# Kernel optimization log

Measured on AMD Instinct MI355X. Metric: run time of the kernel, lower is better.

The kernel has to match this reference:

```python
import jax, jax.numpy as jnp
import numpy as np

D_MODEL = 1024
N_BLOCK = 20
EPS = 1e-8


def setup_inputs() -> dict:
    key = jax.random.key(0)
    k = jax.random.split(key, 7)
    B, S, D, NB = 8, 2048, D_MODEL, N_BLOCK
    e = jax.random.normal(k[0], (B, S, D), dtype=jnp.float32)
    m = jax.random.normal(k[1], (B, S, D), dtype=jnp.float32)
    state = jax.random.normal(k[2], (1, NB * D), dtype=jnp.float32)
    # learned params of the EntNet-style RNN_cell
    U = jax.random.normal(k[3], (D, D), dtype=jnp.float32) * 0.02
    V = jax.random.normal(k[4], (D, D), dtype=jnp.float32) * 0.02
    W = jax.random.normal(k[5], (D, D), dtype=jnp.float32) * 0.02
    keys = jax.random.normal(k[6], (NB, D), dtype=jnp.float32) * 0.02
    return {"e": e, "m": m, "state": state, "U": U, "V": V, "W": W, "keys": keys}


def reference(e, m, state, U, V, W, keys):
    B, S, D = e.shape
    NB = keys.shape[0]
    h0 = state.reshape(NB, D)  # shared initial memory state across batch
    x = e + m  # combined per-timestep input, (B, S, D)

    def step(h, xt):  # h: (NB, D), xt: (D,)
        # per-slot gate: content similarity + key similarity
        g = jax.nn.sigmoid(h @ xt + keys @ xt)  # (NB,)
        # candidate memory
        cand = jnp.tanh(h @ U.T + keys @ V.T + (W @ xt)[None, :])  # (NB, D)
        h = h + g[:, None] * cand
        # per-slot L2 normalization
        h = h / (jnp.linalg.norm(h, axis=1, keepdims=True) + EPS)
        return h, None

    def run(xseq):  # xseq: (S, D) -> final state (NB, D)
        hT, _ = jax.lax.scan(step, h0, xseq)
        return hT

    out = jax.vmap(run)(x)  # (B, NB, D)
    return out
```

## Files before the change

### kernel.cpp

```cpp
#include <hip/hip_runtime.h>
#include <cstdint>
#include <cstddef>

namespace {

constexpr int D   = 1024;
constexpr int NB  = 20;
constexpr int B   = 8;
constexpr int S   = 2048;
constexpr int NWG = 32;
constexpr float EPS = 1e-8f;

typedef __attribute__((ext_vector_type(4))) float f4_t;
typedef __attribute__((ext_vector_type(8))) short s8_t;
typedef unsigned long long u64_t;

__device__ __forceinline__ unsigned short f2bf(float f) {
  unsigned u = __float_as_uint(f);
  u += 0x7fffu + ((u >> 16) & 1u);
  return (unsigned short)(u >> 16);
}
__device__ __forceinline__ float bf2f(unsigned short h) {
  return __uint_as_float(((unsigned)h) << 16);
}
__device__ __forceinline__ float u64lo(u64_t x) { return __uint_as_float((unsigned)x); }
__device__ __forceinline__ float u64hi(u64_t x) { return __uint_as_float((unsigned)(x >> 32)); }
__device__ __forceinline__ float rcp_f(float x) { return __builtin_amdgcn_rcpf(x); }
__device__ __forceinline__ float sigm_fast(float x) { return rcp_f(1.0f + __expf(-x)); }
__device__ __forceinline__ float tanh_fast(float x) {
  const float e = __expf(2.0f * x);
  return 1.0f - 2.0f * rcp_f(e + 1.0f);
}

#define MFMA(a, b, c) __builtin_amdgcn_mfma_f32_16x16x32_bf16((a), (b), (c), 0, 0, 0)
#define ALOAD64(p) __hip_atomic_load((p), __ATOMIC_RELAXED, __HIP_MEMORY_SCOPE_AGENT)
#define ASTORE64(p, v) __hip_atomic_store((p), (v), __ATOMIC_RELAXED, __HIP_MEMORY_SCOPE_AGENT)
#define ALOAD32(p) __hip_atomic_load((p), __ATOMIC_RELAXED, __HIP_MEMORY_SCOPE_AGENT)
#define ASTORE32(p, v) __hip_atomic_store((p), (v), __ATOMIC_RELAXED, __HIP_MEMORY_SCOPE_AGENT)

constexpr size_t OFF_HBUF = 0;
constexpr size_t OFF_NORM = OFF_HBUF + 2ull * B * NB * 512 * 4;
constexpr size_t OFF_CTR  = OFF_NORM + 2ull * B * NB * NWG * 4;
constexpr size_t OFF_KV   = OFF_CTR + (size_t)B * 32 * 4;
constexpr size_t OFF_KX   = OFF_KV + (size_t)NB * D * 4;
constexpr size_t OFF_UHI  = OFF_KX + (size_t)B * S * NB * 4;
constexpr size_t OFF_ULO  = OFF_UHI + (size_t)D * D * 2;
constexpr size_t OFF_WHI  = OFF_ULO + (size_t)D * D * 2;
constexpr size_t OFF_WLO  = OFF_WHI + (size_t)D * D * 2;


__global__ void k_convert(const float* __restrict__ U, const float* __restrict__ W,
                          unsigned short* __restrict__ Uhi, unsigned short* __restrict__ Ulo,
                          unsigned short* __restrict__ Whi, unsigned short* __restrict__ Wlo) {
  const int n = D * D;
  for (int i = blockIdx.x * blockDim.x + threadIdx.x; i < n; i += gridDim.x * blockDim.x) {
    float u = U[i];
    unsigned short h = f2bf(u);
    Uhi[i] = h;
    Ulo[i] = f2bf(u - bf2f(h));
    float w = W[i];
    h = f2bf(w);
    Whi[i] = h;
    Wlo[i] = f2bf(w - bf2f(h));
  }
}

__global__ void k_kv(const float* __restrict__ keys, const float* __restrict__ V,
                     float* __restrict__ KV) {
  const int tid = threadIdx.x;
  const int j = blockIdx.x * 64 + (tid >> 2);
  const int kq = tid & 3;
  const f4_t* v4 = (const f4_t*)(V + (size_t)j * D + kq * 256);
  const f4_t* k4base = (const f4_t*)keys;
  float acc[NB];
#pragma unroll
  for (int i = 0; i < NB; ++i) acc[i] = 0.f;
  for (int q = 0; q < 64; ++q) {
    const f4_t v = v4[q];
#pragma unroll
    for (int i = 0; i < NB; ++i) {
      const f4_t kk = k4base[i * 256 + kq * 64 + q];
      acc[i] += kk[0] * v[0] + kk[1] * v[1] + kk[2] * v[2] + kk[3] * v[3];
    }
  }
#pragma unroll
  for (int i = 0; i < NB; ++i) {
    float s = acc[i];
    s += __shfl_xor(s, 1);
    s += __shfl_xor(s, 2);
    if (kq == 0) KV[(size_t)i * D + j] = s;
  }
}

__global__ void k_kx(const float* __restrict__ e, const float* __restrict__ m,
                     const float* __restrict__ keys, float* __restrict__ KX) {
  __shared__ f4_t xs[256];
  __shared__ float part[NB][8];
  const int bt = blockIdx.x, tid = threadIdx.x;
  xs[tid] = ((const f4_t*)e)[(size_t)bt * 256 + tid] + ((const f4_t*)m)[(size_t)bt * 256 + tid];
  __syncthreads();
  if (tid < 160) {
    const int i = tid >> 3, s8 = tid & 7;
    float acc = 0.f;
    const f4_t* k4 = (const f4_t*)keys + i * 256 + s8 * 32;
    for (int q = 0; q < 32; ++q) {
      const f4_t kk = k4[q];
      const f4_t xx = xs[s8 * 32 + q];
      acc += kk[0] * xx[0] + kk[1] * xx[1] + kk[2] * xx[2] + kk[3] * xx[3];
    }
    part[i][s8] = acc;
  }
  __syncthreads();
  if (tid < NB) {
    float s = 0.f;
#pragma unroll
    for (int q = 0; q < 8; ++q) s += part[tid][q];
    KX[(size_t)bt * NB + tid] = s;
  }
}

__global__ void k_state(const float* __restrict__ state, unsigned* __restrict__ Hbuf,
                        float* __restrict__ NormP, int* __restrict__ ctr) {
  const int idx = blockIdx.x * 256 + threadIdx.x;
  if (idx < B * NB * 512) {
    const int r = idx % (NB * 512);
    const int i = r >> 9, d2 = (r & 511) << 1;
    const unsigned short a = f2bf(state[i * D + d2]);
    const unsigned short c = f2bf(state[i * D + d2 + 1]);
    Hbuf[idx] = (unsigned)a | ((unsigned)c << 16);
  }
  const int j = idx - B * NB * 512;
  if (j >= 0 && j < B * NB * NWG) NormP[j] = 1.0f / 32.0f;
  const int q = idx - B * NB * 512 - B * NB * NWG;
  if (q >= 0 && q < B * 32) ctr[q] = 0;
}


struct __align__(16) LdsT {
  unsigned short hnA[NB * 1024];
  unsigned short xtA[2][1024];
  float credU[4][2][2][16][20];
  float wxAcc[4][2][16];
  float gAcc[4][2][16];
  float KVs[NB][32];
  float ownH[NB][32];
  float pad_force_1_block_per_cu[3072];
};

__device__ __forceinline__ void build_xt(unsigned short* xt , int tid, f4_t x) {
  const unsigned short h0 = f2bf(x[0]), h1 = f2bf(x[1]), h2 = f2bf(x[2]), h3 = f2bf(x[3]);
  const unsigned short u0 = f2bf(x[0] - bf2f(h0)), u1 = f2bf(x[1] - bf2f(h1));
  const unsigned short u2 = f2bf(x[2] - bf2f(h2)), u3 = f2bf(x[3] - bf2f(h3));
  const int kp = tid << 2;
  *(unsigned*)&xt[kp] = (unsigned)h0 | ((unsigned)h1 << 16);
  *(unsigned*)&xt[kp + 2] = (unsigned)h2 | ((unsigned)h3 << 16);
  *(unsigned*)&xt[1024 + kp] = (unsigned)u0 | ((unsigned)u1 << 16);
  *(unsigned*)&xt[1024 + kp + 2] = (unsigned)u2 | ((unsigned)u3 << 16);
}

__device__ __forceinline__ void stage_h(unsigned short* hn, int tid, const u64_t* hv) {
  const int blkk = tid >> 1;
  const int half = (tid & 1) << 2;
#pragma unroll
  for (int j = 0; j < 20; ++j)
    *(u64_t*)&hn[(j << 10) + ((blkk ^ (j & 15)) << 3) + half] = hv[j];
}

__device__ __forceinline__ void bar_lds() {
  asm volatile("s_waitcnt lgkmcnt(0)\n\ts_barrier" ::: "memory");
}
__device__ __forceinline__ void bar_full() {
  asm volatile("s_waitcnt vmcnt(0) lgkmcnt(0)\n\ts_barrier" ::: "memory");
}

__device__ __forceinline__ void poll32(const unsigned* fb, int ln31, int wg,
                                       unsigned tgt, unsigned pv) {
  if (__ballot(pv >= tgt) == ~0ull) return;
  for (;;) {
    const unsigned v = (ln31 == wg) ? tgt : ALOAD32(fb + ln31);
    if (__ballot(v >= tgt) == ~0ull) return;
    __builtin_amdgcn_s_sleep(1);
  }
}

__launch_bounds__(256, 1)
__global__ void k_rnn(const float* __restrict__ e, const float* __restrict__ m,
                      const float* __restrict__ state,
                      const float* __restrict__ KX, const float* __restrict__ KV,
                      const unsigned short* __restrict__ Uhi, const unsigned short* __restrict__ Ulo,
                      const unsigned short* __restrict__ Whi, const unsigned short* __restrict__ Wlo,
                      unsigned* __restrict__ Hbuf, float* __restrict__ NormP,
                      int* __restrict__ ctr, float* __restrict__ out) {
  __shared__ LdsT L;
  const int tid = threadIdx.x;
  const int b = blockIdx.x >> 5;
  const int wg = blockIdx.x & 31;
  const int wv = tid >> 6;
  const int ln = tid & 63;
  const int l15 = ln & 15;
  const int lo4 = ln >> 4;
  const int ln31 = tid & 31;
  unsigned* ctrp = (unsigned*)ctr + b * 32;

  const bool uact = (ln < 40);
  const int ui = wv * 5 + (ln >> 3);
  const int uc4 = (ln & 7) << 2;

  s8_t BUh[2][8], BUl[2][8], BWh[2][8], BWl[2][8];
  {
    const int rowb = (wg << 5) + l15;
#pragma unroll
    for (int nt = 0; nt < 2; ++nt)
#pragma unroll
      for (int kf = 0; kf < 8; ++kf) {
        const size_t off = (size_t)(rowb + nt * 16) * D + (wv << 8) + (kf << 5) + (lo4 << 3);
        BUh[nt][kf] = *(const s8_t*)(Uhi + off);
        BUl[nt][kf] = *(const s8_t*)(Ulo + off);
        BWh[nt][kf] = *(const s8_t*)(Whi + off);
        BWl[nt][kf] = *(const s8_t*)(Wlo + off);
      }
  }
  if (tid < 160) {
    const int i = tid >> 3, c4 = (tid & 7) << 2;
    *(f4_t*)&L.ownH[i][c4] = *(const f4_t*)(state + (size_t)i * D + (wg << 5) + c4);
    *(f4_t*)&L.KVs[i][c4] = *(const f4_t*)(KV + (size_t)i * D + (wg << 5) + c4);
  }

  f4_t evv, mvv;
  float sreg = 1.f;
  float kxreg = 0.f;

  s8_t AX[8];
  f4_t cWa0 = {0, 0, 0, 0}, cWa1 = {0, 0, 0, 0};

  {
    u64_t hv[20];
    const u64_t* hb8 = (const u64_t*)Hbuf + (size_t)(0 * B + b) * (NB * 256);
#pragma unroll
    for (int j = 0; j < 20; ++j) hv[j] = ALOAD64(hb8 + j * 256 + tid);
    const f4_t x0 = ((const f4_t*)e)[(size_t)(b * S) * 256 + tid] +
                    ((const f4_t*)m)[(size_t)(b * S) * 256 + tid];
    build_xt(&L.xtA[0][0], tid, x0);
    stage_h(L.hnA, tid, hv);
    if (uact) kxreg = KX[(size_t)(b * S) * NB + ui];
    evv = ((const f4_t*)e)[(size_t)(b * S + 1) * 256 + tid];
    mvv = ((const f4_t*)m)[(size_t)(b * S + 1) * 256 + tid];
    asm volatile("s_waitcnt lgkmcnt(0)" ::: "memory");
    const unsigned short* xb = &L.xtA[0][0];
#pragma unroll
    for (int kf = 0; kf < 8; ++kf) {
      const int blk = (wv << 5) + (kf << 2) + lo4;
      AX[kf] = *(const s8_t*)&xb[(l15 & 1) * 1024 + (blk << 3)];
    }
#pragma unroll
    for (int kf = 0; kf < 8; ++kf) {
      cWa0 = MFMA(AX[kf], BWh[0][kf], cWa0);
      cWa0 = MFMA(AX[kf], BWl[0][kf], cWa0);
      cWa1 = MFMA(AX[kf], BWh[1][kf], cWa1);
      cWa1 = MFMA(AX[kf], BWl[1][kf], cWa1);
    }
  }
  __syncthreads();

  for (int t = 0; t < S; ++t) {
    const int nxt2 = (t + 1) & 1;

    f4_t cU00 = {0, 0, 0, 0}, cU01 = {0, 0, 0, 0}, cU10 = {0, 0, 0, 0}, cU11 = {0, 0, 0, 0};
    f4_t cG0 = {0, 0, 0, 0}, cG1 = {0, 0, 0, 0};
    {
      const unsigned short* hb = L.hnA;
      const int r1 = 16 + (l15 < 4 ? l15 : 3);
      s8_t A0[8], A1[8];
#pragma unroll
      for (int kf = 0; kf < 8; ++kf) {
        const int blk = (wv << 5) + (kf << 2) + lo4;
        A0[kf] = *(const s8_t*)&hb[(l15 << 10) + ((blk ^ l15) << 3)];
        A1[kf] = *(const s8_t*)&hb[(r1 << 10) + ((blk ^ (r1 & 15)) << 3)];
      }
#pragma unroll
      for (int kf = 0; kf < 8; ++kf) {
        cU00 = MFMA(A0[kf], BUh[0][kf], cU00);
        cU00 = MFMA(A0[kf], BUl[0][kf], cU00);
        cU01 = MFMA(A0[kf], BUh[1][kf], cU01);
        cU01 = MFMA(A0[kf], BUl[1][kf], cU01);
        cU10 = MFMA(A1[kf], BUh[0][kf], cU10);
        cU10 = MFMA(A1[kf], BUl[0][kf], cU10);
        cU11 = MFMA(A1[kf], BUh[1][kf], cU11);
        cU11 = MFMA(A1[kf], BUl[1][kf], cU11);
        cG0 = MFMA(AX[kf], A0[kf], cG0);
        cG1 = MFMA(AX[kf], A1[kf], cG1);
      }
    }
#pragma unroll
    for (int q = 0; q < 4; ++q) {
      const int r = (lo4 << 2) + q;
      L.credU[wv][0][0][r][l15] = cU00[q];
      L.credU[wv][0][1][r][l15] = cU01[q];
      L.credU[wv][1][0][r][l15] = cU10[q];
      L.credU[wv][1][1][r][l15] = cU11[q];
    }
    if (lo4 == 0) {
      L.wxAcc[wv][0][l15] = cWa0[0] + cWa0[1];
      L.wxAcc[wv][1][l15] = cWa1[0] + cWa1[1];
      L.gAcc[wv][0][l15] = cG0[0] + cG0[1];
      L.gAcc[wv][1][l15] = cG1[0] + cG1[1];
    }
    bar_lds();

    unsigned pv = 0;
    if (t + 1 < S) pv = (ln31 == wg) ? (unsigned)(t + 1) : ALOAD32(ctrp + ln31);

    if (uact) {
      const int i = ui, c4 = uc4;
      const int mt = i >> 4, r = i & 15, nt = c4 >> 4, ccc = c4 & 15;
      const f4_t sU = *(const f4_t*)&L.credU[0][mt][nt][r][ccc] +
                      *(const f4_t*)&L.credU[1][mt][nt][r][ccc] +
                      *(const f4_t*)&L.credU[2][mt][nt][r][ccc] +
                      *(const f4_t*)&L.credU[3][mt][nt][r][ccc];
      const f4_t wx = *(const f4_t*)&L.wxAcc[0][nt][ccc] +
                      *(const f4_t*)&L.wxAcc[1][nt][ccc] +
                      *(const f4_t*)&L.wxAcc[2][nt][ccc] +
                      *(const f4_t*)&L.wxAcc[3][nt][ccc];
      const f4_t kv = *(const f4_t*)&L.KVs[i][c4];
      const f4_t oh = *(const f4_t*)&L.ownH[i][c4];
      const float s = sreg;
      const float gpre = s * (L.gAcc[0][mt][r] + L.gAcc[1][mt][r] +
                              L.gAcc[2][mt][r] + L.gAcc[3][mt][r]) + kxreg;
      const float g = sigm_fast(gpre);
      f4_t hn;
      float sq = 0.f;
#pragma unroll
      for (int u = 0; u < 4; ++u) {
        const float cand = tanh_fast(s * sU[u] + kv[u] + wx[u]);
        const float hx = s * oh[u] + g * cand;
        hn[u] = hx;
        sq += hx * hx;
      }
      *(f4_t*)&L.ownH[i][c4] = hn;
      const unsigned d0 = (unsigned)f2bf(hn[0]) | ((unsigned)f2bf(hn[1]) << 16);
      const unsigned d1 = (unsigned)f2bf(hn[2]) | ((unsigned)f2bf(hn[3]) << 16);
      u64_t* hb8 = (u64_t*)Hbuf + (size_t)(nxt2 * B + b) * (NB * 256) +
                   (i << 8) + (wg << 3) + (c4 >> 2);
      ASTORE64(hb8, (u64_t)d0 | ((u64_t)d1 << 32));
      sq += __shfl_xor(sq, 1);
      sq += __shfl_xor(sq, 2);
      sq += __shfl_xor(sq, 4);
      if ((ln & 7) == 0) {
        unsigned* np = (unsigned*)NormP + ((size_t)(nxt2 * B + b) * NB + i) * NWG + wg;
        ASTORE32(np, __float_as_uint(sq));
      }
    }
    bar_full();

    if (tid == 0) ASTORE32(ctrp + wg, (unsigned)(t + 1));

    if (t + 1 < S) {
      poll32(ctrp, ln31, wg, (unsigned)(t + 1), pv);
      u64_t hv[20];
      const u64_t* g0 = (const u64_t*)Hbuf + (size_t)(nxt2 * B + b) * (NB * 256);
#pragma unroll
      for (int j = 0; j < 20; ++j) hv[j] = ALOAD64(g0 + j * 256 + tid);
      float np0 = 0.f;
      if (uact) {
        const u64_t* n0 = (const u64_t*)NormP + ((size_t)(nxt2 * B + b) * NB + ui) * 16 + ((ln & 7) << 1);
        const u64_t a0 = ALOAD64(n0);
        const u64_t a1 = ALOAD64(n0 + 1);
        np0 = u64lo(a0) + u64hi(a0) + u64lo(a1) + u64hi(a1);
        kxreg = KX[((size_t)b * S + t + 1) * NB + ui];
      }
      asm volatile("" ::: "memory");
      build_xt(&L.xtA[0][0], tid, evv + mvv);
      asm volatile("s_waitcnt lgkmcnt(0)" ::: "memory");
      {
        const unsigned short* xb = &L.xtA[0][0];
#pragma unroll
        for (int kf = 0; kf < 8; ++kf) {
          const int blk = (wv << 5) + (kf << 2) + lo4;
          AX[kf] = *(const s8_t*)&xb[(l15 & 1) * 1024 + (blk << 3)];
        }
        cWa0 = (f4_t){0, 0, 0, 0};
        cWa1 = (f4_t){0, 0, 0, 0};
#pragma unroll
        for (int kf = 0; kf < 8; ++kf) {
          cWa0 = MFMA(AX[kf], BWh[0][kf], cWa0);
          cWa0 = MFMA(AX[kf], BWl[0][kf], cWa0);
          cWa1 = MFMA(AX[kf], BWh[1][kf], cWa1);
          cWa1 = MFMA(AX[kf], BWl[1][kf], cWa1);
        }
      }
      stage_h(L.hnA, tid, hv);
      if (t + 2 < S) {
        evv = ((const f4_t*)e)[(size_t)(b * S + t + 2) * 256 + tid];
        mvv = ((const f4_t*)m)[(size_t)(b * S + t + 2) * 256 + tid];
      }
      if (uact) {
        float s0 = np0;
        s0 += __shfl_xor(s0, 1);
        s0 += __shfl_xor(s0, 2);
        s0 += __shfl_xor(s0, 4);
        sreg = rcp_f(sqrtf(s0) + EPS);
      }
    }
    asm volatile("s_waitcnt lgkmcnt(0)" ::: "memory");
  }

  poll32(ctrp, ln31, wg, (unsigned)S, 0u);
  if (uact) {
    const int i = ui, c4 = uc4;
    const u64_t* np8 = (const u64_t*)NormP + ((size_t)(0 * B + b) * NB + i) * 16 + ((ln & 7) << 1);
    const u64_t x0 = ALOAD64(np8);
    const u64_t x1 = ALOAD64(np8 + 1);
    float sq = u64lo(x0) + u64hi(x0) + u64lo(x1) + u64hi(x1);
    sq += __shfl_xor(sq, 1);
    sq += __shfl_xor(sq, 2);
    sq += __shfl_xor(sq, 4);
    const float sc = rcp_f(sqrtf(sq) + EPS);
    const f4_t oh = *(const f4_t*)&L.ownH[i][c4];
    f4_t ov;
#pragma unroll
    for (int u = 0; u < 4; ++u) ov[u] = sc * oh[u];
    *(f4_t*)(out + (size_t)b * NB * D + (size_t)i * D + (wg << 5) + c4) = ov;
  }
}

}

extern "C" void kernel_launch(void* const* d_in, const int* in_sizes, int n_in,
                              void* d_out, int out_size, void* d_ws, size_t ws_size,
                              hipStream_t stream) {
  const float* e = (const float*)d_in[0];
  const float* m = (const float*)d_in[1];
  const float* state = (const float*)d_in[2];
  const float* U = (const float*)d_in[3];
  const float* V = (const float*)d_in[4];
  const float* W = (const float*)d_in[5];
  const float* keys = (const float*)d_in[6];
  float* out = (float*)d_out;
  char* ws = (char*)d_ws;

  unsigned* Hbuf = (unsigned*)(ws + OFF_HBUF);
  float* NormP = (float*)(ws + OFF_NORM);
  int* ctr = (int*)(ws + OFF_CTR);
  float* KV = (float*)(ws + OFF_KV);
  float* KX = (float*)(ws + OFF_KX);
  unsigned short* Uhi = (unsigned short*)(ws + OFF_UHI);
  unsigned short* Ulo = (unsigned short*)(ws + OFF_ULO);
  unsigned short* Whi = (unsigned short*)(ws + OFF_WHI);
  unsigned short* Wlo = (unsigned short*)(ws + OFF_WLO);

  k_convert<<<512, 256, 0, stream>>>(U, W, Uhi, Ulo, Whi, Wlo);
  k_kv<<<16, 256, 0, stream>>>(keys, V, KV);
  k_kx<<<B * S, 256, 0, stream>>>(e, m, keys, KX);
  k_state<<<342, 256, 0, stream>>>(state, Hbuf, NormP, ctr);
  k_rnn<<<B * NWG, 256, 0, stream>>>(e, m, state, KX, KV, Uhi, Ulo, Whi, Wlo,
                                     Hbuf, NormP, ctr, out);
}
```

Before: 11.37 ms.

## Split inter-workgroup polling per wave and hoist gate MFMAs into previous step

Each wave now first waits only on the 8 producer workgroups whose H slices it loads. It then issues those loads and builds x_t and the W·x MFMAs before the full 32-counter poll, which guards the norm partials. The h fragments and the gate MFMAs (x·h) move to the end of the previous iteration and stay in registers, so the next step's LDS reads and gate math come off the critical start of the step. The cost is extra live VGPRs for the kept fragments (register pressure or spills at one wave per SIMD), and ordering now relies on per-wave data partitioning instead of block barriers.

After: 11.50 ms. No clear change (+1.1%).

```diff
diff --git a/kernel.cpp b/kernel.cpp
--- a/kernel.cpp
+++ b/kernel.cpp
@@ -171,6 +171,16 @@
 }
 __device__ __forceinline__ void bar_full() {
   asm volatile("s_waitcnt vmcnt(0) lgkmcnt(0)\n\ts_barrier" ::: "memory");
+}
+
+__device__ __forceinline__ void poll8(const unsigned* fb, int wv, int ln, int wg,
+                                      unsigned tgt) {
+  const int src = (wv << 3) + (ln & 7);
+  for (;;) {
+    const unsigned v = (src == wg) ? tgt : ALOAD32(fb + src);
+    if (__ballot(v >= tgt) == ~0ull) return;
+    __builtin_amdgcn_s_sleep(1);
+  }
 }
 
 __device__ __forceinline__ void poll32(const unsigned* fb, int ln31, int wg,
@@ -200,6 +210,7 @@
   const int l15 = ln & 15;
   const int lo4 = ln >> 4;
   const int ln31 = tid & 31;
+  const int r1 = 16 + (l15 < 4 ? l15 : 3);
   unsigned* ctrp = (unsigned*)ctr + b * 32;
 
   const bool uact = (ln < 40);
@@ -230,8 +241,9 @@
   float sreg = 1.f;
   float kxreg = 0.f;
 
-  s8_t AX[8];
+  s8_t AX[8], A0r[8], A1r[8];
   f4_t cWa0 = {0, 0, 0, 0}, cWa1 = {0, 0, 0, 0};
+  f4_t cGa0 = {0, 0, 0, 0}, cGa1 = {0, 0, 0, 0};
 
   {
     u64_t hv[20];
@@ -247,10 +259,13 @@
     mvv = ((const f4_t*)m)[(size_t)(b * S + 1) * 256 + tid];
     asm volatile("s_waitcnt lgkmcnt(0)" ::: "memory");
     const unsigned short* xb = &L.xtA[0][0];
+    const unsigned short* hb = L.hnA;
 #pragma unroll
     for (int kf = 0; kf < 8; ++kf) {
       const int blk = (wv << 5) + (kf << 2) + lo4;
       AX[kf] = *(const s8_t*)&xb[(l15 & 1) * 1024 + (blk << 3)];
+      A0r[kf] = *(const s8_t*)&hb[(l15 << 10) + ((blk ^ l15) << 3)];
+      A1r[kf] = *(const s8_t*)&hb[(r1 << 10) + ((blk ^ (r1 & 15)) << 3)];
     }
 #pragma unroll
     for (int kf = 0; kf < 8; ++kf) {
@@ -258,6 +273,8 @@
       cWa0 = MFMA(AX[kf], BWl[0][kf], cWa0);
       cWa1 = MFMA(AX[kf], BWh[1][kf], cWa1);
       cWa1 = MFMA(AX[kf], BWl[1][kf], cWa1);
+      cGa0 = MFMA(AX[kf], A0r[kf], cGa0);
+      cGa1 = MFMA(AX[kf], A1r[kf], cGa1);
     }
   }
   __syncthreads();
@@ -266,30 +283,16 @@
     const int nxt2 = (t + 1) & 1;
 
     f4_t cU00 = {0, 0, 0, 0}, cU01 = {0, 0, 0, 0}, cU10 = {0, 0, 0, 0}, cU11 = {0, 0, 0, 0};
-    f4_t cG0 = {0, 0, 0, 0}, cG1 = {0, 0, 0, 0};
-    {
-      const unsigned short* hb = L.hnA;
-      const int r1 = 16 + (l15 < 4 ? l15 : 3);
-      s8_t A0[8], A1[8];
-#pragma unroll
-      for (int kf = 0; kf < 8; ++kf) {
-        const int blk = (wv << 5) + (kf << 2) + lo4;
-        A0[kf] = *(const s8_t*)&hb[(l15 << 10) + ((blk ^ l15) << 3)];
-        A1[kf] = *(const s8_t*)&hb[(r1 << 10) + ((blk ^ (r1 & 15)) << 3)];
-      }
-#pragma unroll
-      for (int kf = 0; kf < 8; ++kf) {
-        cU00 = MFMA(A0[kf], BUh[0][kf], cU00);
-        cU00 = MFMA(A0[kf], BUl[0][kf], cU00);
-        cU01 = MFMA(A0[kf], BUh[1][kf], cU01);
-        cU01 = MFMA(A0[kf], BUl[1][kf], cU01);
-        cU10 = MFMA(A1[kf], BUh[0][kf], cU10);
-        cU10 = MFMA(A1[kf], BUl[0][kf], cU10);
-        cU11 = MFMA(A1[kf], BUh[1][kf], cU11);
-        cU11 = MFMA(A1[kf], BUl[1][kf], cU11);
-        cG0 = MFMA(AX[kf], A0[kf], cG0);
-        cG1 = MFMA(AX[kf], A1[kf], cG1);
-      }
+#pragma unroll
+    for (int kf = 0; kf < 8; ++kf) {
+      cU00 = MFMA(A0r[kf], BUh[0][kf], cU00);
+      cU00 = MFMA(A0r[kf], BUl[0][kf], cU00);
+      cU01 = MFMA(A0r[kf], BUh[1][kf], cU01);
+      cU01 = MFMA(A0r[kf], BUl[1][kf], cU01);
+      cU10 = MFMA(A1r[kf], BUh[0][kf], cU10);
+      cU10 = MFMA(A1r[kf], BUl[0][kf], cU10);
+      cU11 = MFMA(A1r[kf], BUh[1][kf], cU11);
+      cU11 = MFMA(A1r[kf], BUl[1][kf], cU11);
     }
 #pragma unroll
     for (int q = 0; q < 4; ++q) {
@@ -302,8 +305,8 @@
     if (lo4 == 0) {
       L.wxAcc[wv][0][l15] = cWa0[0] + cWa0[1];
       L.wxAcc[wv][1][l15] = cWa1[0] + cWa1[1];
-      L.gAcc[wv][0][l15] = cG0[0] + cG0[1];
-      L.gAcc[wv][1][l15] = cG1[0] + cG1[1];
+      L.gAcc[wv][0][l15] = cGa0[0] + cGa0[1];
+      L.gAcc[wv][1][l15] = cGa1[0] + cGa1[1];
     }
     bar_lds();
 
@@ -355,11 +358,31 @@
     if (tid == 0) ASTORE32(ctrp + wg, (unsigned)(t + 1));
 
     if (t + 1 < S) {
-      poll32(ctrp, ln31, wg, (unsigned)(t + 1), pv);
+      poll8(ctrp, wv, ln, wg, (unsigned)(t + 1));
       u64_t hv[20];
       const u64_t* g0 = (const u64_t*)Hbuf + (size_t)(nxt2 * B + b) * (NB * 256);
 #pragma unroll
       for (int j = 0; j < 20; ++j) hv[j] = ALOAD64(g0 + j * 256 + tid);
+      build_xt(&L.xtA[0][0], tid, evv + mvv);
+      asm volatile("s_waitcnt lgkmcnt(0)" ::: "memory");
+      {
+        const unsigned short* xb = &L.xtA[0][0];
+#pragma unroll
+        for (int kf = 0; kf < 8; ++kf) {
+          const int blk = (wv << 5) + (kf << 2) + lo4;
+          AX[kf] = *(const s8_t*)&xb[(l15 & 1) * 1024 + (blk << 3)];
+        }
+        cWa0 = (f4_t){0, 0, 0, 0};
+        cWa1 = (f4_t){0, 0, 0, 0};
+#pragma unroll
+        for (int kf = 0; kf < 8; ++kf) {
+          cWa0 = MFMA(AX[kf], BWh[0][kf], cWa0);
+          cWa0 = MFMA(AX[kf], BWl[0][kf], cWa0);
+          cWa1 = MFMA(AX[kf], BWh[1][kf], cWa1);
+          cWa1 = MFMA(AX[kf], BWl[1][kf], cWa1);
+        }
+      }
+      poll32(ctrp, ln31, wg, (unsigned)(t + 1), pv);
       float np0 = 0.f;
       if (uact) {
         const u64_t* n0 = (const u64_t*)NormP + ((size_t)(nxt2 * B + b) * NB + ui) * 16 + ((ln & 7) << 1);
@@ -368,30 +391,27 @@
         np0 = u64lo(a0) + u64hi(a0) + u64lo(a1) + u64hi(a1);
         kxreg = KX[((size_t)b * S + t + 1) * NB + ui];
       }
-      asm volatile("" ::: "memory");
-      build_xt(&L.xtA[0][0], tid, evv + mvv);
-      asm volatile("s_waitcnt lgkmcnt(0)" ::: "memory");
-      {
-        const unsigned short* xb = &L.xtA[0][0];
-#pragma unroll
-        for (int kf = 0; kf < 8; ++kf) {
-          const int blk = (wv << 5) + (kf << 2) + lo4;
-          AX[kf] = *(const s8_t*)&xb[(l15 & 1) * 1024 + (blk << 3)];
-        }
-        cWa0 = (f4_t){0, 0, 0, 0};
-        cWa1 = (f4_t){0, 0, 0, 0};
-#pragma unroll
-        for (int kf = 0; kf < 8; ++kf) {
-          cWa0 = MFMA(AX[kf], BWh[0][kf], cWa0);
-          cWa0 = MFMA(AX[kf], BWl[0][kf], cWa0);
-          cWa1 = MFMA(AX[kf], BWh[1][kf], cWa1);
-          cWa1 = MFMA(AX[kf], BWl[1][kf], cWa1);
-        }
-      }
       stage_h(L.hnA, tid, hv);
       if (t + 2 < S) {
         evv = ((const f4_t*)e)[(size_t)(b * S + t + 2) * 256 + tid];
         mvv = ((const f4_t*)m)[(size_t)(b * S + t + 2) * 256 + tid];
+      }
+      asm volatile("s_waitcnt lgkmcnt(0)" ::: "memory");
+      {
+        const unsigned short* hb = L.hnA;
+#pragma unroll
+        for (int kf = 0; kf < 8; ++kf) {
+          const int blk = (wv << 5) + (kf << 2) + lo4;
+          A0r[kf] = *(const s8_t*)&hb[(l15 << 10) + ((blk ^ l15) << 3)];
+          A1r[kf] = *(const s8_t*)&hb[(r1 << 10) + ((blk ^ (r1 & 15)) << 3)];
+        }
+        cGa0 = (f4_t){0, 0, 0, 0};
+        cGa1 = (f4_t){0, 0, 0, 0};
+#pragma unroll
+        for (int kf = 0; kf < 8; ++kf) {
+          cGa0 = MFMA(AX[kf], A0r[kf], cGa0);
+          cGa1 = MFMA(AX[kf], A1r[kf], cGa1);
+        }
       }
       if (uact) {
         float s0 = np0;
@@ -401,7 +421,6 @@
         sreg = rcp_f(sqrtf(s0) + EPS);
       }
     }
-    asm volatile("s_waitcnt lgkmcnt(0)" ::: "memory");
   }
 
   poll32(ctrp, ln31, wg, (unsigned)S, 0u);
```
